# Kernel tuning notes

Hardware: AMD Instinct MI355X
Metric: run time of the kernel (lower is better)

Reference implementation:

```python
import jax, jax.numpy as jnp
import numpy as np

D, NH, HD, L, FF = 768, 12, 64, 2, 3072
EPS = 1e-5
B, F, N = 64, 16, 9


def _ln(x, g, b, eps=EPS):
    m = jnp.mean(x, -1, keepdims=True)
    v = jnp.var(x, -1, keepdims=True)
    return (x - m) * jax.lax.rsqrt(v + eps) * g + b


def _gelu(x):
    return jax.nn.gelu(x, approximate=False)


def _msg_norm(x, msg, scale):
    # torch_geometric MessageNorm: l2-normalize msg, rescale by ||x|| * scale
    msg = msg / jnp.clip(jnp.linalg.norm(msg, axis=-1, keepdims=True), 1e-12)
    return msg * jnp.linalg.norm(x, axis=-1, keepdims=True) * scale


def setup_inputs() -> dict:
    key = jax.random.key(0)
    ks = iter(jax.random.split(key, 64))
    def rn(shape, s=0.02):
        return jax.random.normal(next(ks), shape, jnp.float32) * s
    return dict(
        human_feature=jax.random.normal(next(ks), (B, F, 1, D), jnp.float32),
        obj_features=jax.random.normal(next(ks), (B, F, N, D), jnp.float32),
        edge_features=jax.random.normal(next(ks), (B, F, N, D), jnp.float32),
        # edge_fun: Linear(3D->D), GELU, Linear(D->D), LayerNorm, GELU
        W_e1=rn((3 * D, D)), b_e1=jnp.zeros((D,)),
        W_e2=rn((D, D)), b_e2=jnp.zeros((D,)),
        g_e=jnp.ones((D,)), be_e=jnp.zeros((D,)),
        # message_fun: Linear(2D->D), GELU
        W_m=rn((2 * D, D)), b_m=jnp.zeros((D,)),
        # merging: Linear(D->D), LayerNorm, GELU
        W_mg=rn((D, D)), b_mg=jnp.zeros((D,)),
        g_mg=jnp.ones((D,)), bb_mg=jnp.zeros((D,)),
        # link_fun: Linear(D->1), Sigmoid
        W_l=rn((D, 1)), b_l=jnp.zeros((1,)),
        # MessageNorm learnable scales
        scale_h=jnp.ones(()), scale_o=jnp.ones(()),
        # norm / norm_obj (normtype=5): Linear(D->D), LayerNorm, GELU
        W_nh=rn((D, D)), b_nh=jnp.zeros((D,)), g_nh=jnp.ones((D,)), bb_nh=jnp.zeros((D,)),
        W_no=rn((D, D)), b_no=jnp.zeros((D,)), g_no=jnp.ones((D,)), bb_no=jnp.zeros((D,)),
        # TransformerEncoder, L post-norm layers, stacked over leading axis
        Wqkv=rn((L, D, 3 * D)), bqkv=jnp.zeros((L, 3 * D)),
        Wo_t=rn((L, D, D)), bo_t=jnp.zeros((L, D)),
        g1=jnp.ones((L, D)), bb1=jnp.zeros((L, D)),
        Wf1=rn((L, D, FF)), bf1=jnp.zeros((L, FF)),
        Wf2=rn((L, FF, D)), bf2=jnp.zeros((L, D)),
        g2=jnp.ones((L, D)), bb2=jnp.zeros((L, D)),
    )


def _tfm(x, Wqkv, bqkv, Wo_t, bo_t, g1, bb1, Wf1, bf1, Wf2, bf2, g2, bb2):
    # x: [S, T, D]; post-norm transformer encoder (PyTorch default), GELU FFN
    S, T, _ = x.shape
    scale = 1.0 / jnp.sqrt(jnp.float32(HD))
    for l in range(L):
        qkv = x @ Wqkv[l] + bqkv[l]
        q, k, v = jnp.split(qkv, 3, axis=-1)
        q = q.reshape(S, T, NH, HD)
        k = k.reshape(S, T, NH, HD)
        v = v.reshape(S, T, NH, HD)
        scores = jnp.einsum('sqhd,skhd->shqk', q, k) * scale
        a = jax.nn.softmax(scores, axis=-1)
        o = jnp.einsum('shqk,skhd->sqhd', a, v).reshape(S, T, D)
        x = _ln(x + o @ Wo_t[l] + bo_t[l], g1[l], bb1[l])
        ff = _gelu(x @ Wf1[l] + bf1[l]) @ Wf2[l] + bf2[l]
        x = _ln(x + ff, g2[l], bb2[l])
    return x


def reference(human_feature, obj_features, edge_features,
              W_e1, b_e1, W_e2, b_e2, g_e, be_e,
              W_m, b_m, W_mg, b_mg, g_mg, bb_mg,
              W_l, b_l, scale_h, scale_o,
              W_nh, b_nh, g_nh, bb_nh, W_no, b_no, g_no, bb_no,
              Wqkv, bqkv, Wo_t, bo_t, g1, bb1, Wf1, bf1, Wf2, bf2, g2, bb2):
    B_, F_, N_, D_ = obj_features.shape
    hf = jnp.broadcast_to(human_feature, obj_features.shape)  # repeat over N
    cat = jnp.concatenate([
        jnp.concatenate([hf, edge_features, obj_features], axis=-1),
        jnp.concatenate([obj_features, edge_features, hf], axis=-1)],
        axis=-2)  # [B, F, 2N, 3D]
    h = _gelu(cat @ W_e1 + b_e1)
    h = _gelu(_ln(h @ W_e2 + b_e2, g_e, be_e))  # [B, F, 2N, D]
    # rearrange 'b f n d -> (b n) f d'
    x = h.transpose(0, 2, 1, 3).reshape(B_ * 2 * N_, F_, D_)
    x = _tfm(x, Wqkv, bqkv, Wo_t, bo_t, g1, bb1, Wf1, bf1, Wf2, bf2, g2, bb2)
    tmp_edge = x.reshape(B_, 2 * N_, F_, D_).transpose(0, 2, 1, 3)  # [B,F,2N,D]
    weight_edge = jax.nn.sigmoid(tmp_edge @ W_l + b_l)  # [B,F,2N,1]
    node = jnp.concatenate([hf, obj_features], axis=-2)  # [B,F,2N,D]
    m_v = _gelu(jnp.concatenate([node, tmp_edge], axis=-1) @ W_m + b_m)
    m_v = _gelu(_ln(m_v @ W_mg + b_mg, g_mg, bb_mg))
    ew = weight_edge * m_v
    ewh = jnp.sum(ew[:, :, :N_, :], axis=-2, keepdims=True)  # [B,F,1,D]
    ewo = ew[:, :, N_:, :]                                   # [B,F,N,D]
    h_out = _gelu(_ln((_msg_norm(human_feature, ewh, scale_h) + human_feature) @ W_nh + b_nh, g_nh, bb_nh))
    o_out = _gelu(_ln((_msg_norm(obj_features, ewo, scale_o) + obj_features) @ W_no + b_no, g_no, bb_no))
    return (h_out, o_out)
```

## Files before the change

### kernel.cpp

```cpp
#include <hip/hip_runtime.h>
#include <math.h>

#define DMODEL 768
#define NHEADS 12
#define HEADD  64
#define NLAYERS 2
#define FFD    3072
#define BATCH  64
#define FRAMES 16
#define NOBJ   9
#define TWO_N  (2*NOBJ)
#define ROWS_PER_B (TWO_N*FRAMES)
#define NBF    (BATCH*FRAMES)

typedef float f32x4 __attribute__((ext_vector_type(4)));
typedef short s16x8 __attribute__((ext_vector_type(8)));
typedef unsigned short u16x8 __attribute__((ext_vector_type(8)));

__device__ __forceinline__ float gelu_f(float x) {
    return 0.5f * x * (1.0f + erff(x * 0.70710678118654752440f));
}
__device__ __forceinline__ unsigned short f2bf(float x) {
    unsigned u = __float_as_uint(x);
    unsigned r = (u + 0x7fffu + ((u >> 16) & 1u)) >> 16;
    return (unsigned short)r;
}
__device__ __forceinline__ float bf2f(unsigned short h) {
    return __uint_as_float(((unsigned)h) << 16);
}
__device__ __forceinline__ void store_hl(float v, unsigned short* ph, unsigned short* pl) {
    unsigned short h = f2bf(v);
    *ph = h;
    *pl = f2bf(v - bf2f(h));
}

__global__ __launch_bounds__(256) void wconv_t(
    const float* __restrict__ W, unsigned short* __restrict__ Th,
    unsigned short* __restrict__ Tl, int K, int N)
{
    __shared__ float s[64][65];
    const int k0 = blockIdx.x * 64, n0 = blockIdx.y * 64;
    const int tid = threadIdx.x;
    for (int i = tid; i < 4096; i += 256) {
        int r = i >> 6, c = i & 63;
        s[r][c] = W[(size_t)(k0 + r) * N + n0 + c];
    }
    __syncthreads();
    for (int i = tid; i < 4096; i += 256) {
        int n = i >> 6, k = i & 63;
        float x = s[k][n];
        unsigned short h = f2bf(x);
        size_t o = (size_t)(n0 + n) * K + k0 + k;
        Th[o] = h;
        Tl[o] = f2bf(x - bf2f(h));
    }
}

__global__ __launch_bounds__(256) void gemm_bf16s(
    const unsigned short* __restrict__ Ah, const unsigned short* __restrict__ Al,
    const unsigned short* __restrict__ Bh, const unsigned short* __restrict__ Bl,
    int K, const float* __restrict__ bias,
    float* __restrict__ Cf, unsigned short* __restrict__ Chi,
    unsigned short* __restrict__ Clo,
    int ldc, int M, int act)
{
    __shared__ unsigned short lds[12288];
    const int tid = threadIdx.x;
    const int wid = tid >> 6, l = tid & 63;
    const int row0 = blockIdx.y * 128;
    const int col0 = blockIdx.x * 64;

    const int srow = tid >> 2;
    const int scol = (tid & 3) << 3;
    const size_t ag = (size_t)(row0 + srow) * K + scol;
    const size_t bg = (size_t)(col0 + srow) * K + scol;
    const unsigned short* pAh0 = Ah + ag;
    const unsigned short* pAh1 = Ah + ag + (size_t)64 * K;
    const unsigned short* pAl0 = Al + ag;
    const unsigned short* pAl1 = Al + ag + (size_t)64 * K;
    const unsigned short* pBh  = Bh + bg;
    const unsigned short* pBl  = Bl + bg;
    const int wA0 = srow * 32 + scol;
    const int wA1 = wA0 + 2048;

    const int wr = wid >> 1, wc = wid & 1;
    const int fr = l & 15, fs = l >> 4;
    int aoff[4], boff[2];
    #pragma unroll
    for (int m = 0; m < 4; m++) aoff[m] = (wr * 64 + m * 16 + fr) * 32 + fs * 8;
    #pragma unroll
    for (int n = 0; n < 2; n++) boff[n] = (wc * 32 + n * 16 + fr) * 32 + fs * 8;

    f32x4 acc[4][2];
    #pragma unroll
    for (int m = 0; m < 4; m++)
        #pragma unroll
        for (int n = 0; n < 2; n++) acc[m][n] = (f32x4){0.f, 0.f, 0.f, 0.f};

    u16x8 rah0 = *(const u16x8*)pAh0;
    u16x8 rah1 = *(const u16x8*)pAh1;
    u16x8 ral0 = *(const u16x8*)pAl0;
    u16x8 ral1 = *(const u16x8*)pAl1;
    u16x8 rbh  = *(const u16x8*)pBh;
    u16x8 rbl  = *(const u16x8*)pBl;

    for (int k0 = 0; k0 < K; k0 += 32) {
        __syncthreads();
        *(u16x8*)&lds[wA0]          = rah0;
        *(u16x8*)&lds[wA1]          = rah1;
        *(u16x8*)&lds[4096 + wA0]   = ral0;
        *(u16x8*)&lds[4096 + wA1]   = ral1;
        *(u16x8*)&lds[8192 + wA0]   = rbh;
        *(u16x8*)&lds[10240 + wA0]  = rbl;
        __syncthreads();
        if (k0 + 32 < K) {
            rah0 = *(const u16x8*)(pAh0 + k0 + 32);
            rah1 = *(const u16x8*)(pAh1 + k0 + 32);
            ral0 = *(const u16x8*)(pAl0 + k0 + 32);
            ral1 = *(const u16x8*)(pAl1 + k0 + 32);
            rbh  = *(const u16x8*)(pBh  + k0 + 32);
            rbl  = *(const u16x8*)(pBl  + k0 + 32);
        }
        s16x8 a_h[4], a_l[4], b_h[2], b_l[2];
        #pragma unroll
        for (int m = 0; m < 4; m++) {
            a_h[m] = *(const s16x8*)&lds[aoff[m]];
            a_l[m] = *(const s16x8*)&lds[4096 + aoff[m]];
        }
        #pragma unroll
        for (int n = 0; n < 2; n++) {
            b_h[n] = *(const s16x8*)&lds[8192 + boff[n]];
            b_l[n] = *(const s16x8*)&lds[10240 + boff[n]];
        }
        #pragma unroll
        for (int m = 0; m < 4; m++)
            #pragma unroll
            for (int n = 0; n < 2; n++) {
                acc[m][n] = __builtin_amdgcn_mfma_f32_16x16x32_bf16(a_h[m], b_h[n], acc[m][n], 0, 0, 0);
                acc[m][n] = __builtin_amdgcn_mfma_f32_16x16x32_bf16(a_l[m], b_h[n], acc[m][n], 0, 0, 0);
                acc[m][n] = __builtin_amdgcn_mfma_f32_16x16x32_bf16(a_h[m], b_l[n], acc[m][n], 0, 0, 0);
            }
    }

    #pragma unroll
    for (int n = 0; n < 2; n++) {
        int gcol = col0 + wc * 32 + n * 16 + fr;
        float bv = bias ? bias[gcol] : 0.f;
        #pragma unroll
        for (int m = 0; m < 4; m++) {
            int grow0 = row0 + wr * 64 + m * 16 + (fs << 2);
            #pragma unroll
            for (int j = 0; j < 4; j++) {
                int grow = grow0 + j;
                if (grow < M) {
                    float v = acc[m][n][j] + bv;
                    if (act) v = gelu_f(v);
                    size_t ci = (size_t)grow * ldc + gcol;
                    if (Cf) Cf[ci] = v;
                    if (Chi) store_hl(v, &Chi[ci], &Clo[ci]);
                }
            }
        }
    }
}

__global__ __launch_bounds__(256) void ln_act_f32(
    const float* __restrict__ in, const float* __restrict__ res,
    const float* __restrict__ gamma, const float* __restrict__ beta,
    float* __restrict__ outf, unsigned short* __restrict__ outh,
    unsigned short* __restrict__ outl, int do_gelu)
{
    const int row = blockIdx.x;
    const int tid = threadIdx.x;
    const size_t base = (size_t)row * DMODEL;
    float x0 = in[base + tid];
    float x1 = in[base + tid + 256];
    float x2 = in[base + tid + 512];
    if (res) {
        x0 += res[base + tid];
        x1 += res[base + tid + 256];
        x2 += res[base + tid + 512];
    }
    float s  = x0 + x1 + x2;
    float ss = x0 * x0 + x1 * x1 + x2 * x2;
    #pragma unroll
    for (int o = 32; o > 0; o >>= 1) {
        s  += __shfl_down(s,  o);
        ss += __shfl_down(ss, o);
    }
    __shared__ float sred[4], ssred[4], tot[2];
    const int lane = tid & 63, w = tid >> 6;
    if (lane == 0) { sred[w] = s; ssred[w] = ss; }
    __syncthreads();
    if (tid == 0) {
        tot[0] = sred[0] + sred[1] + sred[2] + sred[3];
        tot[1] = ssred[0] + ssred[1] + ssred[2] + ssred[3];
    }
    __syncthreads();
    const float mean = tot[0] * (1.0f / DMODEL);
    const float var  = tot[1] * (1.0f / DMODEL) - mean * mean;
    const float rstd = rsqrtf(var + 1e-5f);
    #pragma unroll
    for (int rep = 0; rep < 3; rep++) {
        int d = tid + rep * 256;
        float x = (rep == 0) ? x0 : (rep == 1) ? x1 : x2;
        float y = (x - mean) * rstd * gamma[d] + beta[d];
        if (do_gelu) y = gelu_f(y);
        if (outf) outf[base + d] = y;
        if (outh) store_hl(y, &outh[base + d], &outl[base + d]);
    }
}

__global__ __launch_bounds__(256) void attn_k(
    const float* __restrict__ QKV,
    unsigned short* __restrict__ Oh, unsigned short* __restrict__ Ol)
{
    const int blk = blockIdx.x;
    const int h = blk % NHEADS;
    const int s = blk / NHEADS;
    __shared__ float q[16][HEADD], k[16][HEADD], v[16][HEADD], sc[16][17];
    const int tid = threadIdx.x;
    for (int idx = tid; idx < 16 * HEADD; idx += 256) {
        int t = idx >> 6, d = idx & 63;
        size_t base = (size_t)(s * 16 + t) * (3 * DMODEL) + h * HEADD + d;
        q[t][d] = QKV[base];
        k[t][d] = QKV[base + DMODEL];
        v[t][d] = QKV[base + 2 * DMODEL];
    }
    __syncthreads();
    {
        int qt = tid >> 4, kt = tid & 15;
        float a = 0.f;
        #pragma unroll
        for (int d = 0; d < HEADD; d++) a += q[qt][d] * k[kt][d];
        sc[qt][kt] = a * 0.125f;
    }
    __syncthreads();
    if (tid < 16) {
        float m = -1e30f;
        #pragma unroll
        for (int j = 0; j < 16; j++) m = fmaxf(m, sc[tid][j]);
        float sum = 0.f;
        #pragma unroll
        for (int j = 0; j < 16; j++) { float e = expf(sc[tid][j] - m); sc[tid][j] = e; sum += e; }
        float inv = 1.0f / sum;
        #pragma unroll
        for (int j = 0; j < 16; j++) sc[tid][j] *= inv;
    }
    __syncthreads();
    for (int idx = tid; idx < 16 * HEADD; idx += 256) {
        int qt = idx >> 6, d = idx & 63;
        float a = 0.f;
        #pragma unroll
        for (int kt = 0; kt < 16; kt++) a += sc[qt][kt] * v[kt][d];
        size_t o = (size_t)(s * 16 + qt) * DMODEL + h * HEADD + d;
        store_hl(a, &Oh[o], &Ol[o]);
    }
}

__global__ __launch_bounds__(256) void gather_cat1_k(
    const float* __restrict__ hf, const float* __restrict__ obj,
    const float* __restrict__ edge, unsigned short* __restrict__ Qh,
    unsigned short* __restrict__ Ql, int r0)
{
    const int rl = blockIdx.x;
    const int r = r0 + rl;
    const int f = r % FRAMES;
    const int sq = r / FRAMES;
    const int n2 = sq % TWO_N;
    const int b = sq / TWO_N;
    const int bf = b * FRAMES + f;
    const int n = (n2 < NOBJ) ? n2 : (n2 - NOBJ);
    const float* hfp = hf + (size_t)bf * DMODEL;
    const float* edp = edge + ((size_t)bf * NOBJ + n) * DMODEL;
    const float* obp = obj + ((size_t)bf * NOBJ + n) * DMODEL;
    const float* s0 = (n2 < NOBJ) ? hfp : obp;
    const float* s2 = (n2 < NOBJ) ? obp : hfp;
    const size_t ob = (size_t)rl * (3 * DMODEL);
    for (int i = threadIdx.x; i < 3 * DMODEL; i += 256) {
        float v = (i < DMODEL) ? s0[i]
                : (i < 2 * DMODEL) ? edp[i - DMODEL] : s2[i - 2 * DMODEL];
        store_hl(v, &Qh[ob + i], &Ql[ob + i]);
    }
}

__global__ __launch_bounds__(256) void gather_cat2_k(
    const float* __restrict__ hf, const float* __restrict__ obj,
    const unsigned short* __restrict__ Xh, const unsigned short* __restrict__ Xl,
    unsigned short* __restrict__ Qh, unsigned short* __restrict__ Ql, int r0)
{
    const int rl = blockIdx.x;
    const int r = r0 + rl;
    const int f = r % FRAMES;
    const int sq = r / FRAMES;
    const int n2 = sq % TWO_N;
    const int b = sq / TWO_N;
    const int bf = b * FRAMES + f;
    const float* s0 = (n2 < NOBJ)
        ? hf + (size_t)bf * DMODEL
        : obj + ((size_t)bf * NOBJ + (n2 - NOBJ)) * DMODEL;
    const size_t ob = (size_t)rl * (2 * DMODEL);
    const size_t xb = (size_t)rl * DMODEL;
    for (int i = threadIdx.x; i < 2 * DMODEL; i += 256) {
        if (i < DMODEL) {
            store_hl(s0[i], &Qh[ob + i], &Ql[ob + i]);
        } else {
            Qh[ob + i] = Xh[xb + i - DMODEL];
            Ql[ob + i] = Xl[xb + i - DMODEL];
        }
    }
}

__global__ __launch_bounds__(256) void wedge_k(
    const float* __restrict__ X, const float* __restrict__ Wl,
    const float* __restrict__ bl, float* __restrict__ WE)
{
    const int row = blockIdx.x * 4 + (threadIdx.x >> 6);
    const int lane = threadIdx.x & 63;
    const float* xp = X + (size_t)row * DMODEL;
    float a = 0.f;
    #pragma unroll
    for (int i = 0; i < DMODEL / 64; i++)
        a += xp[lane + i * 64] * Wl[lane + i * 64];
    #pragma unroll
    for (int o = 32; o > 0; o >>= 1) a += __shfl_down(a, o);
    if (lane == 0) WE[row] = 1.0f / (1.0f + expf(-(a + bl[0])));
}

__global__ __launch_bounds__(256) void ewh_k(
    const float* __restrict__ MV, const float* __restrict__ WE,
    float* __restrict__ EWH)
{
    const int bfl = blockIdx.x;
    const int bl = bfl / FRAMES, f = bfl % FRAMES;
    const int tid = threadIdx.x;
    #pragma unroll
    for (int rep = 0; rep < 3; rep++) {
        int d = tid + rep * 256;
        float acc = 0.f;
        #pragma unroll
        for (int n2 = 0; n2 < NOBJ; n2++) {
            int rl = (bl * TWO_N + n2) * FRAMES + f;
            acc += WE[rl] * MV[(size_t)rl * DMODEL + d];
        }
        EWH[(size_t)bfl * DMODEL + d] = acc;
    }
}

__global__ __launch_bounds__(256) void buildA_k(
    const float* __restrict__ EWH, const float* __restrict__ MV,
    const float* __restrict__ WE,  const float* __restrict__ hf,
    const float* __restrict__ obj, const float* __restrict__ scale_h,
    const float* __restrict__ scale_o, unsigned short* __restrict__ Ahp,
    unsigned short* __restrict__ Alp, int bf0, int nhuman)
{
    const int row = blockIdx.x;
    const int tid = threadIdx.x;
    const float* msgp; const float* xp; float wsc, sc;
    if (row < nhuman) {
        msgp = EWH + (size_t)row * DMODEL;
        xp   = hf  + (size_t)(bf0 + row) * DMODEL;
        wsc = 1.0f; sc = scale_h[0];
    } else {
        int idx = row - nhuman;
        int n   = idx % NOBJ;
        int bfl = idx / NOBJ;
        int bl = bfl / FRAMES, f = bfl % FRAMES;
        int rl = (bl * TWO_N + NOBJ + n) * FRAMES + f;
        msgp = MV + (size_t)rl * DMODEL;
        xp   = obj + ((size_t)(bf0 + bfl) * NOBJ + n) * DMODEL;
        wsc = WE[rl]; sc = scale_o[0];
    }
    float m0 = msgp[tid]       * wsc;
    float m1 = msgp[tid + 256] * wsc;
    float m2 = msgp[tid + 512] * wsc;
    float x0 = xp[tid], x1 = xp[tid + 256], x2 = xp[tid + 512];
    float sm = m0*m0 + m1*m1 + m2*m2;
    float sx = x0*x0 + x1*x1 + x2*x2;
    #pragma unroll
    for (int o = 32; o > 0; o >>= 1) {
        sm += __shfl_down(sm, o);
        sx += __shfl_down(sx, o);
    }
    __shared__ float smr[4], sxr[4], tot[2];
    const int lane = tid & 63, w = tid >> 6;
    if (lane == 0) { smr[w] = sm; sxr[w] = sx; }
    __syncthreads();
    if (tid == 0) {
        tot[0] = smr[0] + smr[1] + smr[2] + smr[3];
        tot[1] = sxr[0] + sxr[1] + sxr[2] + sxr[3];
    }
    __syncthreads();
    const float nm  = fmaxf(sqrtf(tot[0]), 1e-12f);
    const float fac = sqrtf(tot[1]) * sc / nm;
    const size_t ob = (size_t)row * DMODEL;
    store_hl(m0 * fac + x0, &Ahp[ob + tid],       &Alp[ob + tid]);
    store_hl(m1 * fac + x1, &Ahp[ob + tid + 256], &Alp[ob + tid + 256]);
    store_hl(m2 * fac + x2, &Ahp[ob + tid + 512], &Alp[ob + tid + 512]);
}

extern "C" void kernel_launch(void* const* d_in, const int* in_sizes, int n_in,
                              void* d_out, int out_size, void* d_ws, size_t ws_size,
                              hipStream_t stream)
{
    const float* hf   = (const float*)d_in[0];
    const float* obj  = (const float*)d_in[1];
    const float* edge = (const float*)d_in[2];
    const float* W_e1 = (const float*)d_in[3];
    const float* b_e1 = (const float*)d_in[4];
    const float* W_e2 = (const float*)d_in[5];
    const float* b_e2 = (const float*)d_in[6];
    const float* g_e  = (const float*)d_in[7];
    const float* be_e = (const float*)d_in[8];
    const float* W_m  = (const float*)d_in[9];
    const float* b_m  = (const float*)d_in[10];
    const float* W_mg = (const float*)d_in[11];
    const float* b_mg = (const float*)d_in[12];
    const float* g_mg = (const float*)d_in[13];
    const float* bb_mg= (const float*)d_in[14];
    const float* W_l  = (const float*)d_in[15];
    const float* b_l  = (const float*)d_in[16];
    const float* scale_h = (const float*)d_in[17];
    const float* scale_o = (const float*)d_in[18];
    const float* W_nh = (const float*)d_in[19];
    const float* b_nh = (const float*)d_in[20];
    const float* g_nh = (const float*)d_in[21];
    const float* bb_nh= (const float*)d_in[22];
    const float* W_no = (const float*)d_in[23];
    const float* b_no = (const float*)d_in[24];
    const float* g_no = (const float*)d_in[25];
    const float* bb_no= (const float*)d_in[26];
    const float* Wqkv = (const float*)d_in[27];
    const float* bqkv = (const float*)d_in[28];
    const float* Wo_t = (const float*)d_in[29];
    const float* bo_t = (const float*)d_in[30];
    const float* g1   = (const float*)d_in[31];
    const float* bb1  = (const float*)d_in[32];
    const float* Wf1  = (const float*)d_in[33];
    const float* bf1  = (const float*)d_in[34];
    const float* Wf2  = (const float*)d_in[35];
    const float* bf2  = (const float*)d_in[36];
    const float* g2   = (const float*)d_in[37];
    const float* bb2  = (const float*)d_in[38];

    float* out = (float*)d_out;
    unsigned short* wts = (unsigned short*)d_ws;

    size_t wo = 0;
    auto alloc2 = [&](size_t n, unsigned short** h, unsigned short** l) {
        *h = wts + wo; *l = wts + wo + n; wo += 2 * n;
    };
    unsigned short *we1h,*we1l,*we2h,*we2l,*wmh,*wml,*wmgh,*wmgl,*wnhh,*wnhl,*wnoh,*wnol;
    unsigned short *qkvh[2],*qkvl[2],*woh[2],*wol[2],*wf1h[2],*wf1l[2],*wf2h[2],*wf2l[2];
    alloc2((size_t)768*2304, &we1h, &we1l);
    alloc2((size_t)768*768,  &we2h, &we2l);
    alloc2((size_t)768*1536, &wmh,  &wml);
    alloc2((size_t)768*768,  &wmgh, &wmgl);
    alloc2((size_t)768*768,  &wnhh, &wnhl);
    alloc2((size_t)768*768,  &wnoh, &wnol);
    for (int l = 0; l < 2; l++) {
        alloc2((size_t)2304*768, &qkvh[l], &qkvl[l]);
        alloc2((size_t)768*768,  &woh[l],  &wol[l]);
        alloc2((size_t)3072*768, &wf1h[l], &wf1l[l]);
        alloc2((size_t)768*3072, &wf2h[l], &wf2l[l]);
    }
    const size_t wbytes = wo * sizeof(unsigned short);

    wconv_t<<<dim3(2304/64, 768/64), 256, 0, stream>>>(W_e1, we1h, we1l, 2304, 768);
    wconv_t<<<dim3(768/64,  768/64), 256, 0, stream>>>(W_e2, we2h, we2l, 768, 768);
    wconv_t<<<dim3(1536/64, 768/64), 256, 0, stream>>>(W_m,  wmh,  wml,  1536, 768);
    wconv_t<<<dim3(768/64,  768/64), 256, 0, stream>>>(W_mg, wmgh, wmgl, 768, 768);
    wconv_t<<<dim3(768/64,  768/64), 256, 0, stream>>>(W_nh, wnhh, wnhl, 768, 768);
    wconv_t<<<dim3(768/64,  768/64), 256, 0, stream>>>(W_no, wnoh, wnol, 768, 768);
    for (int l = 0; l < 2; l++) {
        wconv_t<<<dim3(768/64, 2304/64), 256, 0, stream>>>(Wqkv + (size_t)l*768*2304, qkvh[l], qkvl[l], 768, 2304);
        wconv_t<<<dim3(768/64,  768/64), 256, 0, stream>>>(Wo_t + (size_t)l*768*768,  woh[l],  wol[l],  768, 768);
        wconv_t<<<dim3(768/64, 3072/64), 256, 0, stream>>>(Wf1  + (size_t)l*768*3072, wf1h[l], wf1l[l], 768, 3072);
        wconv_t<<<dim3(3072/64, 768/64), 256, 0, stream>>>(Wf2  + (size_t)l*3072*768, wf2h[l], wf2l[l], 3072, 768);
    }

    const size_t avail = ws_size - wbytes;
    int CB = 4;
    {
        const int cands[5] = {64, 32, 16, 8, 4};
        for (int i = 0; i < 5; i++) {
            size_t R = (size_t)cands[i] * ROWS_PER_B;
            size_t need = R * 27652 + (size_t)cands[i] * 49152 + 8192;
            if (need <= avail) { CB = cands[i]; break; }
        }
    }
    const int R = CB * ROWS_PER_B;
    const int nhuman = CB * FRAMES;
    const int nobjr  = CB * FRAMES * NOBJ;

    char* base = (char*)(wts + wo);
    float* Qbig = (float*)base;
    float* X    = Qbig + (size_t)R * 2304;
    unsigned short* Xh = (unsigned short*)(X + (size_t)R * DMODEL);
    unsigned short* Xl = Xh + (size_t)R * DMODEL;
    unsigned short* Yh = Xl + (size_t)R * DMODEL;
    unsigned short* Yl = Yh + (size_t)R * FFD;
    float* EWH = (float*)(Yl + (size_t)R * FFD);
    float* WE  = EWH + (size_t)nhuman * DMODEL;
    float* Z  = Qbig;
    float* MV = Qbig + (size_t)R * DMODEL;
    unsigned short* Q1h = (unsigned short*)Qbig;
    unsigned short* Q1l = Q1h + (size_t)R * 2304;
    unsigned short* Q2h = (unsigned short*)Qbig;
    unsigned short* Q2l = Q2h + (size_t)R * 1536;

    auto G = [&](const unsigned short* Ah, const unsigned short* Al, int K,
                 const unsigned short* Bh, const unsigned short* Bl,
                 const float* bias, float* Cf, unsigned short* Chi,
                 unsigned short* Clo, int ldc, int M, int N, int act) {
        dim3 grid(N / 64, (M + 127) / 128);
        gemm_bf16s<<<grid, 256, 0, stream>>>(Ah, Al, Bh, Bl, K, bias,
                                             Cf, Chi, Clo, ldc, M, act);
    };

    for (int b0 = 0; b0 < BATCH; b0 += CB) {
        const int r0  = b0 * ROWS_PER_B;
        const int bf0 = b0 * FRAMES;

        gather_cat1_k<<<R, 256, 0, stream>>>(hf, obj, edge, Q1h, Q1l, r0);
        G(Q1h, Q1l, 2304, we1h, we1l, b_e1, nullptr, Yh, Yl, 768, R, 768, 1);
        G(Yh, Yl, 768, we2h, we2l, b_e2, Z, nullptr, nullptr, 768, R, 768, 0);
        ln_act_f32<<<R, 256, 0, stream>>>(Z, nullptr, g_e, be_e, X, Xh, Xl, 1);

        for (int l = 0; l < NLAYERS; l++) {
            G(Xh, Xl, 768, qkvh[l], qkvl[l], bqkv + (size_t)l * 2304,
              Qbig, nullptr, nullptr, 2304, R, 2304, 0);
            attn_k<<<(R / 16) * NHEADS, 256, 0, stream>>>(Qbig, Yh, Yl);
            G(Yh, Yl, 768, woh[l], wol[l], bo_t + (size_t)l * 768,
              Z, nullptr, nullptr, 768, R, 768, 0);
            ln_act_f32<<<R, 256, 0, stream>>>(Z, X, g1 + l*DMODEL, bb1 + l*DMODEL, X, Xh, Xl, 0);
            G(Xh, Xl, 768, wf1h[l], wf1l[l], bf1 + (size_t)l * FFD,
              nullptr, Yh, Yl, FFD, R, FFD, 1);
            G(Yh, Yl, FFD, wf2h[l], wf2l[l], bf2 + (size_t)l * 768,
              Z, nullptr, nullptr, 768, R, 768, 0);
            ln_act_f32<<<R, 256, 0, stream>>>(Z, X, g2 + l*DMODEL, bb2 + l*DMODEL, X, Xh, Xl, 0);
        }

        wedge_k<<<R / 4, 256, 0, stream>>>(X, W_l, b_l, WE);
        gather_cat2_k<<<R, 256, 0, stream>>>(hf, obj, Xh, Xl, Q2h, Q2l, r0);
        G(Q2h, Q2l, 1536, wmh, wml, b_m, nullptr, Yh, Yl, 768, R, 768, 1);
        G(Yh, Yl, 768, wmgh, wmgl, b_mg, Z, nullptr, nullptr, 768, R, 768, 0);
        ln_act_f32<<<R, 256, 0, stream>>>(Z, nullptr, g_mg, bb_mg, MV, nullptr, nullptr, 1);
        ewh_k<<<nhuman, 256, 0, stream>>>(MV, WE, EWH);
        buildA_k<<<nhuman + nobjr, 256, 0, stream>>>(EWH, MV, WE, hf, obj,
                                                     scale_h, scale_o, Xh, Xl, bf0, nhuman);
        G(Xh, Xl, 768, wnhh, wnhl, b_nh, Z, nullptr, nullptr, 768, nhuman, 768, 0);
        G(Xh + (size_t)nhuman*DMODEL, Xl + (size_t)nhuman*DMODEL, 768, wnoh, wnol,
          b_no, Z + (size_t)nhuman*DMODEL, nullptr, nullptr, 768, nobjr, 768, 0);
        ln_act_f32<<<nhuman, 256, 0, stream>>>(Z, nullptr, g_nh, bb_nh,
                                               out + (size_t)bf0 * DMODEL, nullptr, nullptr, 1);
        ln_act_f32<<<nobjr, 256, 0, stream>>>(Z + (size_t)nhuman*DMODEL, nullptr,
                                              g_no, bb_no,
                                              out + (size_t)NBF*DMODEL + (size_t)bf0*NOBJ*DMODEL,
                                              nullptr, nullptr, 1);
    }
}
```

Measured before the change: 4.499 ms.

## Shrink workspace: split FFN into accumulated halves, store QKV/residual as bf16 pairs

The FFN is split into two 1536-wide chunks. The second FF2 GEMM accumulates into the fp32 output through a new accum flag. QKV and the residual stream are now kept only as hi/lo bf16 pairs instead of fp32, and the GEMM gets an XCD-aware block-id swizzle. Together these cut the per-row workspace so a larger batch chunk can fit, which means fewer chunk iterations and less memory traffic. The cost is an extra read-modify-write of Z and more GEMM launches.

Result: faster. 4.098 ms (-8.9%).

```diff
diff --git a/kernel.cpp b/kernel.cpp
--- a/kernel.cpp
+++ b/kernel.cpp
@@ -16,27 +16,28 @@
 typedef float f32x4 __attribute__((ext_vector_type(4)));
 typedef short s16x8 __attribute__((ext_vector_type(8)));
 typedef unsigned short u16x8 __attribute__((ext_vector_type(8)));
+typedef unsigned short u16;
 
 __device__ __forceinline__ float gelu_f(float x) {
     return 0.5f * x * (1.0f + erff(x * 0.70710678118654752440f));
 }
-__device__ __forceinline__ unsigned short f2bf(float x) {
+__device__ __forceinline__ u16 f2bf(float x) {
     unsigned u = __float_as_uint(x);
     unsigned r = (u + 0x7fffu + ((u >> 16) & 1u)) >> 16;
-    return (unsigned short)r;
-}
-__device__ __forceinline__ float bf2f(unsigned short h) {
+    return (u16)r;
+}
+__device__ __forceinline__ float bf2f(u16 h) {
     return __uint_as_float(((unsigned)h) << 16);
 }
-__device__ __forceinline__ void store_hl(float v, unsigned short* ph, unsigned short* pl) {
-    unsigned short h = f2bf(v);
+__device__ __forceinline__ void store_hl(float v, u16* ph, u16* pl) {
+    u16 h = f2bf(v);
     *ph = h;
     *pl = f2bf(v - bf2f(h));
 }
 
 __global__ __launch_bounds__(256) void wconv_t(
-    const float* __restrict__ W, unsigned short* __restrict__ Th,
-    unsigned short* __restrict__ Tl, int K, int N)
+    const float* __restrict__ W, u16* __restrict__ Th,
+    u16* __restrict__ Tl, int K, int N)
 {
     __shared__ float s[64][65];
     const int k0 = blockIdx.x * 64, n0 = blockIdx.y * 64;
@@ -49,7 +50,7 @@
     for (int i = tid; i < 4096; i += 256) {
         int n = i >> 6, k = i & 63;
         float x = s[k][n];
-        unsigned short h = f2bf(x);
+        u16 h = f2bf(x);
         size_t o = (size_t)(n0 + n) * K + k0 + k;
         Th[o] = h;
         Tl[o] = f2bf(x - bf2f(h));
@@ -57,29 +58,32 @@
 }
 
 __global__ __launch_bounds__(256) void gemm_bf16s(
-    const unsigned short* __restrict__ Ah, const unsigned short* __restrict__ Al,
-    const unsigned short* __restrict__ Bh, const unsigned short* __restrict__ Bl,
+    const u16* __restrict__ Ah, const u16* __restrict__ Al,
+    const u16* __restrict__ Bh, const u16* __restrict__ Bl,
     int K, const float* __restrict__ bias,
-    float* __restrict__ Cf, unsigned short* __restrict__ Chi,
-    unsigned short* __restrict__ Clo,
-    int ldc, int M, int act)
-{
-    __shared__ unsigned short lds[12288];
+    float* __restrict__ Cf, u16* __restrict__ Chi, u16* __restrict__ Clo,
+    int ldc, int M, int act, int accum)
+{
+    __shared__ u16 lds[12288];
     const int tid = threadIdx.x;
     const int wid = tid >> 6, l = tid & 63;
-    const int row0 = blockIdx.y * 128;
-    const int col0 = blockIdx.x * 64;
+
+    int nwg = gridDim.x * gridDim.y;
+    int bid = blockIdx.y * gridDim.x + blockIdx.x;
+    if ((nwg & 7) == 0) bid = (bid & 7) * (nwg >> 3) + (bid >> 3);
+    const int col0 = (bid % gridDim.x) * 64;
+    const int row0 = (bid / gridDim.x) * 128;
 
     const int srow = tid >> 2;
     const int scol = (tid & 3) << 3;
     const size_t ag = (size_t)(row0 + srow) * K + scol;
     const size_t bg = (size_t)(col0 + srow) * K + scol;
-    const unsigned short* pAh0 = Ah + ag;
-    const unsigned short* pAh1 = Ah + ag + (size_t)64 * K;
-    const unsigned short* pAl0 = Al + ag;
-    const unsigned short* pAl1 = Al + ag + (size_t)64 * K;
-    const unsigned short* pBh  = Bh + bg;
-    const unsigned short* pBl  = Bl + bg;
+    const u16* pAh0 = Ah + ag;
+    const u16* pAh1 = Ah + ag + (size_t)64 * K;
+    const u16* pAl0 = Al + ag;
+    const u16* pAl1 = Al + ag + (size_t)64 * K;
+    const u16* pBh  = Bh + bg;
+    const u16* pBl  = Bl + bg;
     const int wA0 = srow * 32 + scol;
     const int wA1 = wA0 + 2048;
 
@@ -156,6 +160,7 @@
                     float v = acc[m][n][j] + bv;
                     if (act) v = gelu_f(v);
                     size_t ci = (size_t)grow * ldc + gcol;
+                    if (accum) v += Cf[ci];
                     if (Cf) Cf[ci] = v;
                     if (Chi) store_hl(v, &Chi[ci], &Clo[ci]);
                 }
@@ -164,11 +169,12 @@
     }
 }
 
-__global__ __launch_bounds__(256) void ln_act_f32(
-    const float* __restrict__ in, const float* __restrict__ res,
+__global__ __launch_bounds__(256) void ln_act(
+    const float* __restrict__ in, const u16* __restrict__ resH,
+    const u16* __restrict__ resL,
     const float* __restrict__ gamma, const float* __restrict__ beta,
-    float* __restrict__ outf, unsigned short* __restrict__ outh,
-    unsigned short* __restrict__ outl, int do_gelu)
+    float* __restrict__ outF, u16* __restrict__ outH, u16* __restrict__ outL,
+    int do_gelu)
 {
     const int row = blockIdx.x;
     const int tid = threadIdx.x;
@@ -176,10 +182,10 @@
     float x0 = in[base + tid];
     float x1 = in[base + tid + 256];
     float x2 = in[base + tid + 512];
-    if (res) {
-        x0 += res[base + tid];
-        x1 += res[base + tid + 256];
-        x2 += res[base + tid + 512];
+    if (resH) {
+        x0 += bf2f(resH[base + tid])       + bf2f(resL[base + tid]);
+        x1 += bf2f(resH[base + tid + 256]) + bf2f(resL[base + tid + 256]);
+        x2 += bf2f(resH[base + tid + 512]) + bf2f(resL[base + tid + 512]);
     }
     float s  = x0 + x1 + x2;
     float ss = x0 * x0 + x1 * x1 + x2 * x2;
@@ -206,14 +212,14 @@
         float x = (rep == 0) ? x0 : (rep == 1) ? x1 : x2;
         float y = (x - mean) * rstd * gamma[d] + beta[d];
         if (do_gelu) y = gelu_f(y);
-        if (outf) outf[base + d] = y;
-        if (outh) store_hl(y, &outh[base + d], &outl[base + d]);
+        if (outF) outF[base + d] = y;
+        if (outH) store_hl(y, &outH[base + d], &outL[base + d]);
     }
 }
 
 __global__ __launch_bounds__(256) void attn_k(
-    const float* __restrict__ QKV,
-    unsigned short* __restrict__ Oh, unsigned short* __restrict__ Ol)
+    const u16* __restrict__ Qh, const u16* __restrict__ Ql,
+    u16* __restrict__ Oh, u16* __restrict__ Ol)
 {
     const int blk = blockIdx.x;
     const int h = blk % NHEADS;
@@ -223,9 +229,9 @@
     for (int idx = tid; idx < 16 * HEADD; idx += 256) {
         int t = idx >> 6, d = idx & 63;
         size_t base = (size_t)(s * 16 + t) * (3 * DMODEL) + h * HEADD + d;
-        q[t][d] = QKV[base];
-        k[t][d] = QKV[base + DMODEL];
-        v[t][d] = QKV[base + 2 * DMODEL];
+        q[t][d] = bf2f(Qh[base])              + bf2f(Ql[base]);
+        k[t][d] = bf2f(Qh[base + DMODEL])     + bf2f(Ql[base + DMODEL]);
+        v[t][d] = bf2f(Qh[base + 2 * DMODEL]) + bf2f(Ql[base + 2 * DMODEL]);
     }
     __syncthreads();
     {
@@ -260,8 +266,8 @@
 
 __global__ __launch_bounds__(256) void gather_cat1_k(
     const float* __restrict__ hf, const float* __restrict__ obj,
-    const float* __restrict__ edge, unsigned short* __restrict__ Qh,
-    unsigned short* __restrict__ Ql, int r0)
+    const float* __restrict__ edge, u16* __restrict__ Qh,
+    u16* __restrict__ Ql, int r0)
 {
     const int rl = blockIdx.x;
     const int r = r0 + rl;
@@ -286,8 +292,8 @@
 
 __global__ __launch_bounds__(256) void gather_cat2_k(
     const float* __restrict__ hf, const float* __restrict__ obj,
-    const unsigned short* __restrict__ Xh, const unsigned short* __restrict__ Xl,
-    unsigned short* __restrict__ Qh, unsigned short* __restrict__ Ql, int r0)
+    const u16* __restrict__ Xh, const u16* __restrict__ Xl,
+    u16* __restrict__ Qh, u16* __restrict__ Ql, int r0)
 {
     const int rl = blockIdx.x;
     const int r = r0 + rl;
@@ -312,16 +318,19 @@
 }
 
 __global__ __launch_bounds__(256) void wedge_k(
-    const float* __restrict__ X, const float* __restrict__ Wl,
-    const float* __restrict__ bl, float* __restrict__ WE)
+    const u16* __restrict__ Xh, const u16* __restrict__ Xl,
+    const float* __restrict__ Wl, const float* __restrict__ bl,
+    float* __restrict__ WE)
 {
     const int row = blockIdx.x * 4 + (threadIdx.x >> 6);
     const int lane = threadIdx.x & 63;
-    const float* xp = X + (size_t)row * DMODEL;
+    const size_t base = (size_t)row * DMODEL;
     float a = 0.f;
     #pragma unroll
-    for (int i = 0; i < DMODEL / 64; i++)
-        a += xp[lane + i * 64] * Wl[lane + i * 64];
+    for (int i = 0; i < DMODEL / 64; i++) {
+        int d = lane + i * 64;
+        a += (bf2f(Xh[base + d]) + bf2f(Xl[base + d])) * Wl[d];
+    }
     #pragma unroll
     for (int o = 32; o > 0; o >>= 1) a += __shfl_down(a, o);
     if (lane == 0) WE[row] = 1.0f / (1.0f + expf(-(a + bl[0])));
@@ -351,8 +360,8 @@
     const float* __restrict__ EWH, const float* __restrict__ MV,
     const float* __restrict__ WE,  const float* __restrict__ hf,
     const float* __restrict__ obj, const float* __restrict__ scale_h,
-    const float* __restrict__ scale_o, unsigned short* __restrict__ Ahp,
-    unsigned short* __restrict__ Alp, int bf0, int nhuman)
+    const float* __restrict__ scale_o, u16* __restrict__ Ahp,
+    u16* __restrict__ Alp, int bf0, int nhuman)
 {
     const int row = blockIdx.x;
     const int tid = threadIdx.x;
@@ -444,14 +453,14 @@
     const float* bb2  = (const float*)d_in[38];
 
     float* out = (float*)d_out;
-    unsigned short* wts = (unsigned short*)d_ws;
+    u16* wts = (u16*)d_ws;
 
     size_t wo = 0;
-    auto alloc2 = [&](size_t n, unsigned short** h, unsigned short** l) {
+    auto alloc2 = [&](size_t n, u16** h, u16** l) {
         *h = wts + wo; *l = wts + wo + n; wo += 2 * n;
     };
-    unsigned short *we1h,*we1l,*we2h,*we2l,*wmh,*wml,*wmgh,*wmgl,*wnhh,*wnhl,*wnoh,*wnol;
-    unsigned short *qkvh[2],*qkvl[2],*woh[2],*wol[2],*wf1h[2],*wf1l[2],*wf2h[2],*wf2l[2];
+    u16 *we1h,*we1l,*we2h,*we2l,*wmh,*wml,*wmgh,*wmgl,*wnhh,*wnhl,*wnoh,*wnol;
+    u16 *qkvh[2],*qkvl[2],*woh[2],*wol[2],*wf1h[2],*wf1l[2],*wf2h[2],*wf2l[2];
     alloc2((size_t)768*2304, &we1h, &we1l);
     alloc2((size_t)768*768,  &we2h, &we2l);
     alloc2((size_t)768*1536, &wmh,  &wml);
@@ -464,7 +473,7 @@
         alloc2((size_t)3072*768, &wf1h[l], &wf1l[l]);
         alloc2((size_t)768*3072, &wf2h[l], &wf2l[l]);
     }
-    const size_t wbytes = wo * sizeof(unsigned short);
+    const size_t wbytes = wo * sizeof(u16);
 
     wconv_t<<<dim3(2304/64, 768/64), 256, 0, stream>>>(W_e1, we1h, we1l, 2304, 768);
     wconv_t<<<dim3(768/64,  768/64), 256, 0, stream>>>(W_e2, we2h, we2l, 768, 768);
@@ -476,7 +485,12 @@
         wconv_t<<<dim3(768/64, 2304/64), 256, 0, stream>>>(Wqkv + (size_t)l*768*2304, qkvh[l], qkvl[l], 768, 2304);
         wconv_t<<<dim3(768/64,  768/64), 256, 0, stream>>>(Wo_t + (size_t)l*768*768,  woh[l],  wol[l],  768, 768);
         wconv_t<<<dim3(768/64, 3072/64), 256, 0, stream>>>(Wf1  + (size_t)l*768*3072, wf1h[l], wf1l[l], 768, 3072);
-        wconv_t<<<dim3(3072/64, 768/64), 256, 0, stream>>>(Wf2  + (size_t)l*3072*768, wf2h[l], wf2l[l], 3072, 768);
+        for (int c = 0; c < 2; c++) {
+            wconv_t<<<dim3(1536/64, 768/64), 256, 0, stream>>>(
+                Wf2 + (size_t)l*3072*768 + (size_t)c*1536*768,
+                wf2h[l] + (size_t)c*768*1536, wf2l[l] + (size_t)c*768*1536,
+                1536, 768);
+        }
     }
 
     const size_t avail = ws_size - wbytes;
@@ -485,7 +499,7 @@
         const int cands[5] = {64, 32, 16, 8, 4};
         for (int i = 0; i < 5; i++) {
             size_t R = (size_t)cands[i] * ROWS_PER_B;
-            size_t need = R * 27652 + (size_t)cands[i] * 49152 + 8192;
+            size_t need = R * 18436 + (size_t)cands[i] * 49152 + 65536;
             if (need <= avail) { CB = cands[i]; break; }
         }
     }
@@ -493,70 +507,75 @@
     const int nhuman = CB * FRAMES;
     const int nobjr  = CB * FRAMES * NOBJ;
 
-    char* base = (char*)(wts + wo);
-    float* Qbig = (float*)base;
-    float* X    = Qbig + (size_t)R * 2304;
-    unsigned short* Xh = (unsigned short*)(X + (size_t)R * DMODEL);
-    unsigned short* Xl = Xh + (size_t)R * DMODEL;
-    unsigned short* Yh = Xl + (size_t)R * DMODEL;
-    unsigned short* Yl = Yh + (size_t)R * FFD;
-    float* EWH = (float*)(Yl + (size_t)R * FFD);
+    u16* Xh = wts + wo;
+    u16* Xl = Xh + (size_t)R * DMODEL;
+    u16* Yh = Xl + (size_t)R * DMODEL;
+    u16* Yl = Yh + (size_t)R * 1536;
+    char* QKVZ = (char*)(Yl + (size_t)R * 1536);
+    float* EWH = (float*)(QKVZ + (size_t)R * 9216);
     float* WE  = EWH + (size_t)nhuman * DMODEL;
-    float* Z  = Qbig;
-    float* MV = Qbig + (size_t)R * DMODEL;
-    unsigned short* Q1h = (unsigned short*)Qbig;
-    unsigned short* Q1l = Q1h + (size_t)R * 2304;
-    unsigned short* Q2h = (unsigned short*)Qbig;
-    unsigned short* Q2l = Q2h + (size_t)R * 1536;
-
-    auto G = [&](const unsigned short* Ah, const unsigned short* Al, int K,
-                 const unsigned short* Bh, const unsigned short* Bl,
-                 const float* bias, float* Cf, unsigned short* Chi,
-                 unsigned short* Clo, int ldc, int M, int N, int act) {
+    u16* Qbh = (u16*)QKVZ;
+    u16* Qbl = Qbh + (size_t)R * 2304;
+    u16* Q2h = (u16*)QKVZ;
+    u16* Q2l = Q2h + (size_t)R * 1536;
+    float* Z  = (float*)QKVZ;
+    float* MV = (float*)Yh;
+
+    auto G = [&](const u16* Ah, const u16* Al, int K,
+                 const u16* Bh, const u16* Bl, const float* bias,
+                 float* Cf, u16* Chi, u16* Clo, int ldc, int M, int N,
+                 int act, int accum) {
         dim3 grid(N / 64, (M + 127) / 128);
         gemm_bf16s<<<grid, 256, 0, stream>>>(Ah, Al, Bh, Bl, K, bias,
-                                             Cf, Chi, Clo, ldc, M, act);
+                                             Cf, Chi, Clo, ldc, M, act, accum);
     };
 
     for (int b0 = 0; b0 < BATCH; b0 += CB) {
         const int r0  = b0 * ROWS_PER_B;
         const int bf0 = b0 * FRAMES;
 
-        gather_cat1_k<<<R, 256, 0, stream>>>(hf, obj, edge, Q1h, Q1l, r0);
-        G(Q1h, Q1l, 2304, we1h, we1l, b_e1, nullptr, Yh, Yl, 768, R, 768, 1);
-        G(Yh, Yl, 768, we2h, we2l, b_e2, Z, nullptr, nullptr, 768, R, 768, 0);
-        ln_act_f32<<<R, 256, 0, stream>>>(Z, nullptr, g_e, be_e, X, Xh, Xl, 1);
+        gather_cat1_k<<<R, 256, 0, stream>>>(hf, obj, edge, Qbh, Qbl, r0);
+        G(Qbh, Qbl, 2304, we1h, we1l, b_e1, nullptr, Yh, Yl, 768, R, 768, 1, 0);
+        G(Yh, Yl, 768, we2h, we2l, b_e2, Z, nullptr, nullptr, 768, R, 768, 0, 0);
+        ln_act<<<R, 256, 0, stream>>>(Z, nullptr, nullptr, g_e, be_e,
+                                      nullptr, Xh, Xl, 1);
 
         for (int l = 0; l < NLAYERS; l++) {
             G(Xh, Xl, 768, qkvh[l], qkvl[l], bqkv + (size_t)l * 2304,
-              Qbig, nullptr, nullptr, 2304, R, 2304, 0);
-            attn_k<<<(R / 16) * NHEADS, 256, 0, stream>>>(Qbig, Yh, Yl);
+              nullptr, Qbh, Qbl, 2304, R, 2304, 0, 0);
+            attn_k<<<(R / 16) * NHEADS, 256, 0, stream>>>(Qbh, Qbl, Yh, Yl);
             G(Yh, Yl, 768, woh[l], wol[l], bo_t + (size_t)l * 768,
-              Z, nullptr, nullptr, 768, R, 768, 0);
-            ln_act_f32<<<R, 256, 0, stream>>>(Z, X, g1 + l*DMODEL, bb1 + l*DMODEL, X, Xh, Xl, 0);
-            G(Xh, Xl, 768, wf1h[l], wf1l[l], bf1 + (size_t)l * FFD,
-              nullptr, Yh, Yl, FFD, R, FFD, 1);
-            G(Yh, Yl, FFD, wf2h[l], wf2l[l], bf2 + (size_t)l * 768,
-              Z, nullptr, nullptr, 768, R, 768, 0);
-            ln_act_f32<<<R, 256, 0, stream>>>(Z, X, g2 + l*DMODEL, bb2 + l*DMODEL, X, Xh, Xl, 0);
-        }
-
-        wedge_k<<<R / 4, 256, 0, stream>>>(X, W_l, b_l, WE);
+              Z, nullptr, nullptr, 768, R, 768, 0, 0);
+            ln_act<<<R, 256, 0, stream>>>(Z, Xh, Xl, g1 + l*DMODEL, bb1 + l*DMODEL,
+                                          nullptr, Xh, Xl, 0);
+            for (int c = 0; c < 2; c++) {
+                G(Xh, Xl, 768, wf1h[l] + (size_t)c*1536*768, wf1l[l] + (size_t)c*1536*768,
+                  bf1 + (size_t)l*FFD + c*1536, nullptr, Yh, Yl, 1536, R, 1536, 1, 0);
+                G(Yh, Yl, 1536, wf2h[l] + (size_t)c*768*1536, wf2l[l] + (size_t)c*768*1536,
+                  (c == 0 ? bf2 + (size_t)l*768 : nullptr), Z, nullptr, nullptr,
+                  768, R, 768, 0, (c > 0) ? 1 : 0);
+            }
+            ln_act<<<R, 256, 0, stream>>>(Z, Xh, Xl, g2 + l*DMODEL, bb2 + l*DMODEL,
+                                          nullptr, Xh, Xl, 0);
+        }
+
+        wedge_k<<<R / 4, 256, 0, stream>>>(Xh, Xl, W_l, b_l, WE);
         gather_cat2_k<<<R, 256, 0, stream>>>(hf, obj, Xh, Xl, Q2h, Q2l, r0);
-        G(Q2h, Q2l, 1536, wmh, wml, b_m, nullptr, Yh, Yl, 768, R, 768, 1);
-        G(Yh, Yl, 768, wmgh, wmgl, b_mg, Z, nullptr, nullptr, 768, R, 768, 0);
-        ln_act_f32<<<R, 256, 0, stream>>>(Z, nullptr, g_mg, bb_mg, MV, nullptr, nullptr, 1);
+        G(Q2h, Q2l, 1536, wmh, wml, b_m, nullptr, Yh, Yl, 768, R, 768, 1, 0);
+        G(Yh, Yl, 768, wmgh, wmgl, b_mg, Z, nullptr, nullptr, 768, R, 768, 0, 0);
+        ln_act<<<R, 256, 0, stream>>>(Z, nullptr, nullptr, g_mg, bb_mg,
+                                      MV, nullptr, nullptr, 1);
         ewh_k<<<nhuman, 256, 0, stream>>>(MV, WE, EWH);
         buildA_k<<<nhuman + nobjr, 256, 0, stream>>>(EWH, MV, WE, hf, obj,
                                                      scale_h, scale_o, Xh, Xl, bf0, nhuman);
-        G(Xh, Xl, 768, wnhh, wnhl, b_nh, Z, nullptr, nullptr, 768, nhuman, 768, 0);
+        G(Xh, Xl, 768, wnhh, wnhl, b_nh, Z, nullptr, nullptr, 768, nhuman, 768, 0, 0);
         G(Xh + (size_t)nhuman*DMODEL, Xl + (size_t)nhuman*DMODEL, 768, wnoh, wnol,
-          b_no, Z + (size_t)nhuman*DMODEL, nullptr, nullptr, 768, nobjr, 768, 0);
-        ln_act_f32<<<nhuman, 256, 0, stream>>>(Z, nullptr, g_nh, bb_nh,
-                                               out + (size_t)bf0 * DMODEL, nullptr, nullptr, 1);
-        ln_act_f32<<<nobjr, 256, 0, stream>>>(Z + (size_t)nhuman*DMODEL, nullptr,
-                                              g_no, bb_no,
-                                              out + (size_t)NBF*DMODEL + (size_t)bf0*NOBJ*DMODEL,
-                                              nullptr, nullptr, 1);
-    }
-}
+          b_no, Z + (size_t)nhuman*DMODEL, nullptr, nullptr, 768, nobjr, 768, 0, 0);
+        ln_act<<<nhuman, 256, 0, stream>>>(Z, nullptr, nullptr, g_nh, bb_nh,
+                                           out + (size_t)bf0 * DMODEL, nullptr, nullptr, 1);
+        ln_act<<<nobjr, 256, 0, stream>>>(Z + (size_t)nhuman*DMODEL, nullptr, nullptr,
+                                          g_no, bb_no,
+                                          out + (size_t)NBF*DMODEL + (size_t)bf0*NOBJ*DMODEL,
+                                          nullptr, nullptr, 1);
+    }
+}
```
